# Optimization experiments

Measured on AMD Instinct MI355X. Metric: run time of the kernel, lower is better.

Reference implementation:

```python
import jax, jax.numpy as jnp
import numpy as np

N_RAYS = 65536
N_SAMPLES = 96


def setup_inputs() -> dict:
    key = jax.random.key(0)
    k1, k2, k3 = jax.random.split(key, 3)
    rgb = jax.random.uniform(k1, (N_RAYS, N_SAMPLES, 3), dtype=jnp.float32)
    # SDF values near the surface, small magnitude
    sdf = jax.random.normal(k2, (N_RAYS, N_SAMPLES), dtype=jnp.float32) * 0.1
    # monotonically increasing sample depths along each ray
    z_vals = jnp.sort(
        jax.random.uniform(k3, (N_RAYS, N_SAMPLES), dtype=jnp.float32,
                           minval=0.1, maxval=5.0), axis=-1)
    return {"rgb": rgb, "sdf": sdf, "z_vals": z_vals, "beta": 10}


def reference(rgb, sdf, z_vals, beta):
    # sdf2alpha: alpha = 1 - exp(-beta * sigmoid(-sdf * beta))
    alpha = 1.0 - jnp.exp(-beta * jax.nn.sigmoid(-sdf * beta))  # [N, S]
    # exclusive cumprod of (1 - alpha + 1e-10): transmittance
    trans = jnp.cumprod(
        jnp.concatenate([jnp.ones_like(alpha[:, :1]), 1.0 - alpha + 1e-10],
                        axis=-1), axis=-1)[:, :-1]  # [N, S]
    weights = alpha * trans  # [N, S]
    rendered_rgb = jnp.sum(weights[..., None] * rgb, axis=-2)  # [N, 3]
    rendered_depth = jnp.sum(weights * z_vals, axis=-1)  # [N]
    return (rendered_depth, rendered_rgb, sdf, z_vals)
```

## Files before the change

kernel.cpp:

```cpp
#include <hip/hip_runtime.h>


#define SDFR_NS 96
#define SDFR_RPB 32

struct f3 { float x, y, z; };

__device__ __forceinline__ void compute_ray(
    int l, float beta,
    const f3& sv, const f3& zv, const f3& ca, const f3& cb, const f3& cc,
    float& depth, float& r0, float& r1, float& r2)
{
    const float e0 = __expf(-beta * __builtin_amdgcn_rcpf(1.0f + __expf(sv.x * beta)));
    const float e1 = __expf(-beta * __builtin_amdgcn_rcpf(1.0f + __expf(sv.y * beta)));
    const float e2 = __expf(-beta * __builtin_amdgcn_rcpf(1.0f + __expf(sv.z * beta)));
    const float a0 = 1.0f - e0, t0 = e0 + 1e-10f;
    const float a1 = 1.0f - e1, t1 = e1 + 1e-10f;
    const float a2 = 1.0f - e2, t2 = e2 + 1e-10f;

    float scan = t0 * t1 * t2;
    #pragma unroll
    for (int d = 1; d < 32; d <<= 1) {
        float v = __shfl_up(scan, d, 32);
        if (l >= d) scan *= v;
    }
    float E = __shfl_up(scan, 1, 32);
    if (l == 0) E = 1.0f;

    const float w0 = a0 * E;
    const float w1 = a1 * E * t0;
    const float w2 = a2 * E * t0 * t1;

    depth = w0 * zv.x + w1 * zv.y + w2 * zv.z;
    r0    = w0 * ca.x + w1 * cb.x + w2 * cc.x;
    r1    = w0 * ca.y + w1 * cb.y + w2 * cc.y;
    r2    = w0 * ca.z + w1 * cb.z + w2 * cc.z;

    #pragma unroll
    for (int d = 16; d >= 1; d >>= 1) {
        depth += __shfl_xor(depth, d, 32);
        r0    += __shfl_xor(r0, d, 32);
        r1    += __shfl_xor(r1, d, 32);
        r2    += __shfl_xor(r2, d, 32);
    }
}

__global__ __launch_bounds__(256, 4) void sdf_render_kernel(
    const float* __restrict__ rgb,
    const float* __restrict__ sdf,
    const float* __restrict__ z_vals,
    const int*   __restrict__ beta_p,
    float* __restrict__ out_depth,
    float* __restrict__ out_rgb,
    float* __restrict__ out_sdf,
    float* __restrict__ out_z,
    int n_rays)
{
    const int t    = threadIdx.x;
    const int g    = t >> 5;
    const int l    = t & 31;
    const int base = blockIdx.x * SDFR_RPB;

    int bi = *beta_p;
    float beta;
    if (bi > 1000000 || bi < -1000000) {
        union { int i; float f; } u; u.i = bi; beta = u.f;
    } else {
        beta = (float)bi;
    }

    f3 sv0, zv0, ca0, cb0, cc0;
    f3 sv1, zv1, ca1, cb1, cc1;
    f3 sv2, zv2, ca2, cb2, cc2;
    f3 sv3, zv3, ca3, cb3, cc3;

#define SDFR_LOAD(K, RAY)                                           \
    do {                                                            \
        const int sb_ = (RAY) * SDFR_NS + 3 * l;                    \
        const int rb_ = (RAY) * (SDFR_NS * 3) + 9 * l;              \
        sv##K = *(const f3*)(sdf    + sb_);                         \
        zv##K = *(const f3*)(z_vals + sb_);                         \
        ca##K = *(const f3*)(rgb + rb_ + 0);                        \
        cb##K = *(const f3*)(rgb + rb_ + 3);                        \
        cc##K = *(const f3*)(rgb + rb_ + 6);                        \
    } while (0)

#define SDFR_PASS(K, RAY)                                           \
    do {                                                            \
        const int sb_ = (RAY) * SDFR_NS + 3 * l;                    \
        *(f3*)(out_sdf + sb_) = sv##K;                              \
        *(f3*)(out_z   + sb_) = zv##K;                              \
    } while (0)

#define SDFR_RUN(K, RAY)                                            \
    do {                                                            \
        float d_, x_, y_, w_;                                       \
        compute_ray(l, beta, sv##K, zv##K, ca##K, cb##K, cc##K,     \
                    d_, x_, y_, w_);                                \
        if (l == 0) {                                               \
            out_depth[(RAY)] = d_;                                  \
            f3 o_; o_.x = x_; o_.y = y_; o_.z = w_;                 \
            *(f3*)(out_rgb + (RAY) * 3) = o_;                       \
        }                                                           \
    } while (0)

    if (base + SDFR_RPB <= n_rays) {
        const int r0_ = base + g;
        const int r1_ = r0_ + 8;
        const int r2_ = r0_ + 16;
        const int r3_ = r0_ + 24;

        SDFR_LOAD(0, r0_);
        SDFR_LOAD(1, r1_);
        SDFR_LOAD(2, r2_);
        SDFR_LOAD(3, r3_);
        __builtin_amdgcn_sched_barrier(0);

        SDFR_PASS(0, r0_);
        SDFR_RUN(0, r0_);
        SDFR_PASS(1, r1_);
        SDFR_RUN(1, r1_);
        SDFR_PASS(2, r2_);
        SDFR_RUN(2, r2_);
        SDFR_PASS(3, r3_);
        SDFR_RUN(3, r3_);
    } else {
        for (int p = 0; p < 4; ++p) {
            const int ray = base + p * 8 + g;
            if (ray < n_rays) {
                SDFR_LOAD(0, ray);
                SDFR_PASS(0, ray);
                SDFR_RUN(0, ray);
            }
        }
    }

#undef SDFR_LOAD
#undef SDFR_PASS
#undef SDFR_RUN
}

extern "C" void kernel_launch(void* const* d_in, const int* in_sizes, int n_in,
                              void* d_out, int out_size, void* d_ws, size_t ws_size,
                              hipStream_t stream) {
    (void)n_in; (void)d_ws; (void)ws_size; (void)out_size;

    const float* rgb    = (const float*)d_in[0];
    const float* sdf    = (const float*)d_in[1];
    const float* z      = (const float*)d_in[2];
    const int*   beta_p = (const int*)d_in[3];

    const int n_rays = in_sizes[1] / SDFR_NS;

    float* out_depth = (float*)d_out;
    float* out_rgb   = out_depth + n_rays;
    float* out_sdf   = out_rgb   + (size_t)n_rays * 3;
    float* out_z     = out_sdf   + (size_t)n_rays * SDFR_NS;

    const int grid = (n_rays + SDFR_RPB - 1) / SDFR_RPB;
    sdf_render_kernel<<<grid, 256, 0, stream>>>(
        rgb, sdf, z, beta_p, out_depth, out_rgb, out_sdf, out_z, n_rays);
}
```

Measured before the change: 170.2 us.

## Split sdf/z passthrough copy into separate vectorized nontemporal copy kernel

Removes the passthrough stores of sdf and z_vals from the compute kernel and adds a second grid-stride kernel that copies them with float4 loads and nontemporal stores. Inline asm pins the loaded registers so the compute kernel still issues all loads up front. The intent is to get fully coalesced 16-byte traffic for the copy instead of strided 12-byte stores, at the cost of re-reading sdf and z from memory (possibly from cache) and a second launch.

```diff
diff --git a/kernel.cpp b/kernel.cpp
--- a/kernel.cpp
+++ b/kernel.cpp
@@ -5,6 +5,7 @@
 #define SDFR_RPB 32
 
 struct f3 { float x, y, z; };
+typedef float fv4 __attribute__((ext_vector_type(4)));
 
 __device__ __forceinline__ void compute_ray(
     int l, float beta,
@@ -45,15 +46,13 @@
     }
 }
 
-__global__ __launch_bounds__(256, 4) void sdf_render_kernel(
+__global__ __launch_bounds__(256, 4) void sdf_compute_kernel(
     const float* __restrict__ rgb,
     const float* __restrict__ sdf,
     const float* __restrict__ z_vals,
     const int*   __restrict__ beta_p,
     float* __restrict__ out_depth,
     float* __restrict__ out_rgb,
-    float* __restrict__ out_sdf,
-    float* __restrict__ out_z,
     int n_rays)
 {
     const int t    = threadIdx.x;
@@ -85,12 +84,13 @@
         cc##K = *(const f3*)(rgb + rb_ + 6);                        \
     } while (0)
 
-#define SDFR_PASS(K, RAY)                                           \
-    do {                                                            \
-        const int sb_ = (RAY) * SDFR_NS + 3 * l;                    \
-        *(f3*)(out_sdf + sb_) = sv##K;                              \
-        *(f3*)(out_z   + sb_) = zv##K;                              \
-    } while (0)
+#define SDFR_PIN(K)                                                 \
+    asm volatile("" :                                               \
+        "+v"(sv##K.x), "+v"(sv##K.y), "+v"(sv##K.z),                \
+        "+v"(zv##K.x), "+v"(zv##K.y), "+v"(zv##K.z),                \
+        "+v"(ca##K.x), "+v"(ca##K.y), "+v"(ca##K.z),                \
+        "+v"(cb##K.x), "+v"(cb##K.y), "+v"(cb##K.z),                \
+        "+v"(cc##K.x), "+v"(cc##K.y), "+v"(cc##K.z))
 
 #define SDFR_RUN(K, RAY)                                            \
     do {                                                            \
@@ -116,28 +116,52 @@
         SDFR_LOAD(3, r3_);
         __builtin_amdgcn_sched_barrier(0);
 
-        SDFR_PASS(0, r0_);
+        SDFR_PIN(0);
+        SDFR_PIN(1);
+        SDFR_PIN(2);
+        SDFR_PIN(3);
+
         SDFR_RUN(0, r0_);
-        SDFR_PASS(1, r1_);
         SDFR_RUN(1, r1_);
-        SDFR_PASS(2, r2_);
         SDFR_RUN(2, r2_);
-        SDFR_PASS(3, r3_);
         SDFR_RUN(3, r3_);
     } else {
         for (int p = 0; p < 4; ++p) {
             const int ray = base + p * 8 + g;
             if (ray < n_rays) {
                 SDFR_LOAD(0, ray);
-                SDFR_PASS(0, ray);
                 SDFR_RUN(0, ray);
             }
         }
     }
 
 #undef SDFR_LOAD
-#undef SDFR_PASS
+#undef SDFR_PIN
 #undef SDFR_RUN
+}
+
+#define SDFR_CPB 2048
+
+__global__ __launch_bounds__(256, 8) void sdf_copy_kernel(
+    const float* __restrict__ sdf,
+    const float* __restrict__ z_vals,
+    float* __restrict__ out_sdf,
+    float* __restrict__ out_z,
+    int n_rays)
+{
+    const int n4     = (n_rays * SDFR_NS) / 4;
+    const int stride = SDFR_CPB * 256;
+    const fv4* __restrict__ s4 = (const fv4*)sdf;
+    const fv4* __restrict__ z4 = (const fv4*)z_vals;
+    fv4* __restrict__ os4 = (fv4*)out_sdf;
+    fv4* __restrict__ oz4 = (fv4*)out_z;
+
+    for (int i = blockIdx.x * 256 + threadIdx.x; i < n4; i += stride) {
+        const fv4 a = s4[i];
+        const fv4 b = z4[i];
+        __builtin_nontemporal_store(a, os4 + i);
+        __builtin_nontemporal_store(b, oz4 + i);
+    }
 }
 
 extern "C" void kernel_launch(void* const* d_in, const int* in_sizes, int n_in,
@@ -157,7 +181,10 @@
     float* out_sdf   = out_rgb   + (size_t)n_rays * 3;
     float* out_z     = out_sdf   + (size_t)n_rays * SDFR_NS;
 
-    const int grid = (n_rays + SDFR_RPB - 1) / SDFR_RPB;
-    sdf_render_kernel<<<grid, 256, 0, stream>>>(
-        rgb, sdf, z, beta_p, out_depth, out_rgb, out_sdf, out_z, n_rays);
+    const int comp_blocks = (n_rays + SDFR_RPB - 1) / SDFR_RPB;
+    sdf_compute_kernel<<<comp_blocks, 256, 0, stream>>>(
+        rgb, sdf, z, beta_p, out_depth, out_rgb, n_rays);
+
+    sdf_copy_kernel<<<SDFR_CPB, 256, 0, stream>>>(
+        sdf, z, out_sdf, out_z, n_rays);
 }
```

New measurement: 179.0 us. +5.1%, slower.
